# Optimization experiments

Hardware: AMD Instinct MI355X
Metric: run time of the kernel (lower is better)

## Reference

```python
import jax, jax.numpy as jnp
import numpy as np

EPS = 1e-18
MARGIN = 0.2  # hp.margin (cancels: positive/positive == 1)
BIAS = 1.0    # hp.bias


def setup_inputs() -> dict:
    key = jax.random.key(0)
    k1, k2, k3, k4 = jax.random.split(key, 4)
    B, T, D = 32, 256, 256  # T == D required by the broadcast in Ecos_sim
    return {
        "pre_VF": jax.random.normal(k1, (B, T, D), dtype=jnp.float32),
        "pre_AF": jax.random.normal(k2, (B, T, D), dtype=jnp.float32),
        "back_VF": jax.random.normal(k3, (B, T, D), dtype=jnp.float32),
        "back_AF": jax.random.normal(k4, (B, T, D), dtype=jnp.float32),
    }


def _direction_loss(V, A):
    """For each anchor i: log(1 + sum_{j != i} exp(sim(V_i, A_j))).

    sim(V_i, A_j)[t, s] = (V_i @ A_j.T)[t, s] / (||V_i||_F * colnorm(A_j)[s])
    (faithful to Ecos_sim: scalar Frobenius norm for V, per-column norm for A,
    broadcast along the last axis; positive/positive == 1 exactly, so the
    positive term and margin cancel.)
    """
    B = V.shape[0]
    # upper[i,j,t,s] = <V[i,t,:], A[j,s,:]>
    upper = jnp.einsum("itd,jsd->ijts", V, A)
    v_norm = jnp.sqrt(jnp.sum(V ** 2, axis=(1, 2)) + EPS)      # [B]
    a_norm = jnp.sqrt(jnp.sum(A ** 2, axis=1) + EPS)           # [B, D]
    sim = upper / (v_norm[:, None, None, None] * a_norm[None, :, None, :])
    e_sim = jnp.exp(sim)                                        # [B,B,T,T]
    idx = jnp.arange(B)
    down = e_sim.sum(axis=1) - e_sim[idx, idx]                  # exclude j == i
    rows = jnp.log(1.0 + down)                                  # [B,T,T]
    return rows.reshape(-1, rows.shape[-1])                     # cat along dim 0


def reference(pre_VF, pre_AF, back_VF, back_AF):
    sim_back_V = _direction_loss(back_VF, back_AF)
    sim_back_A = _direction_loss(back_AF, back_VF)
    return -(1.0 / BIAS) * (sim_back_V + sim_back_A)
```

## Files before the change

kernel.cpp:

```cpp
#include <hip/hip_runtime.h>
#include <cstdint>

#define R_TOT 8192
#define KD    256
#define SLOT  ((size_t)R_TOT * KD)
#define IVN_OFF  0
#define ICN_OFF  256
#define CSQ_OFF  (ICN_OFF + 65536)
#define MATS_OFF (CSQ_OFF + 524288)

typedef float f32x4 __attribute__((ext_vector_type(4)));
typedef long  lx2   __attribute__((ext_vector_type(2)));

__device__ __forceinline__ void glds16(const void* g, void* l){
  __builtin_amdgcn_global_load_lds((const __attribute__((address_space(1))) uint32_t*)g,
                                   (__attribute__((address_space(3))) uint32_t*)l, 16, 0, 0);
}

__global__ void cast_ns_k(const float* __restrict__ V, const float* __restrict__ A,
                          unsigned char* __restrict__ mats, float* __restrict__ csq){
  const int tc = blockIdx.x, j = blockIdx.y, ten = blockIdx.z;
  const int tid = threadIdx.x;
  const int g    = tid & 31;
  const int tsub = tid >> 5;
  const int q    = ((g >> 3) << 2) | (g & 3);
  const int half = (g >> 2) & 1;
  const float* X = (ten ? A : V) + (size_t)j * 65536;
  unsigned char* M = mats + (size_t)ten * SLOT + (size_t)j * 65536;
  float cs[8];
  #pragma unroll
  for (int e = 0; e < 8; ++e) cs[e] = 0.f;
  #pragma unroll
  for (int tt = 0; tt < 4; ++tt){
    const int t = tc * 32 + tt * 8 + tsub;
    const float4 p0 = *(const float4*)(X + t * 256 + g * 8);
    const float4 p1 = *(const float4*)(X + t * 256 + g * 8 + 4);
    cs[0] += p0.x * p0.x; cs[1] += p0.y * p0.y; cs[2] += p0.z * p0.z; cs[3] += p0.w * p0.w;
    cs[4] += p1.x * p1.x; cs[5] += p1.y * p1.y; cs[6] += p1.z * p1.z; cs[7] += p1.w * p1.w;
    int d0 = __builtin_amdgcn_cvt_pk_fp8_f32(p0.x, p0.y, 0, false);
    d0     = __builtin_amdgcn_cvt_pk_fp8_f32(p0.z, p0.w, d0, true);
    int d1 = __builtin_amdgcn_cvt_pk_fp8_f32(p1.x, p1.y, 0, false);
    d1     = __builtin_amdgcn_cvt_pk_fp8_f32(p1.z, p1.w, d1, true);
    int2 o; o.x = d0; o.y = d1;
    *(int2*)(M + (size_t)t * 256 + (((q ^ (t & 15)) << 4) | (half << 3))) = o;
  }
  __shared__ float red[8][256];
  #pragma unroll
  for (int e = 0; e < 8; ++e) red[tsub][g * 8 + e] = cs[e];
  __syncthreads();
  float s = 0.f;
  #pragma unroll
  for (int gg = 0; gg < 8; ++gg) s += red[gg][tid];
  csq[(size_t)((tc * 2 + ten) * 32 + j) * 256 + tid] = s;
}

__global__ void nreduce_k(const float* __restrict__ csq, float* __restrict__ ivn,
                          float* __restrict__ icn){
  const int j = blockIdx.x, ten = blockIdx.y, s = threadIdx.x;
  float c = 0.f;
  #pragma unroll
  for (int tc = 0; tc < 8; ++tc)
    c += csq[(size_t)((tc * 2 + ten) * 32 + j) * 256 + s];
  icn[ten * 8192 + j * 256 + s] = rsqrtf(c + 1e-18f);
  __shared__ float red[256];
  red[s] = c; __syncthreads();
  for (int off = 128; off > 0; off >>= 1){
    if (s < off) red[s] += red[s + off];
    __syncthreads();
  }
  if (s == 0) ivn[ten * 32 + j] = rsqrtf(red[0] + 1e-18f);
}

__global__ __launch_bounds__(256, 4) void gemm_both_k(const unsigned char* __restrict__ mats,
                                                      const float* __restrict__ ivn,
                                                      const float* __restrict__ icn,
                                                      float* __restrict__ out){
  __shared__ __align__(16) char smem[16384];
  const int tid  = threadIdx.x;
  const int lane = tid & 63;
  const int w    = tid >> 6;
  const int wm   = (w & 1) * 32;
  const int wn   = (w >> 1) * 16;
  const int wno  = wn << 8;
  const int lm   = lane & 15;
  const int kh   = lane >> 4;
  const int s0   = blockIdx.x * 32;
  const int rb   = blockIdx.y;
  const int r0   = rb * 64;
  const int ib   = rb >> 2;

  int a4[4];
  {
    const int base  = lm * 256 + ((kh ^ (lm & 3)) << 4);
    const int base2 = base ^ ((lm >> 2) << 6);
    #pragma unroll
    for (int t = 0; t < 4; ++t) a4[t] = base2 ^ (t << 6);
  }

  f32x4 accd[2][2];
  #pragma unroll
  for (int d = 0; d < 2; ++d)
    #pragma unroll
    for (int mi = 0; mi < 2; ++mi)
      accd[d][mi] = f32x4{0.f, 0.f, 0.f, 0.f};

  #pragma unroll
  for (int dir = 0; dir < 2; ++dir){
    const unsigned char* rowmat = mats + (size_t)dir * SLOT;
    const unsigned char* colmat = mats + (size_t)(1 - dir) * SLOT;
    const float sivn = ivn[dir * 32 + ib] * 1.44269504088896340736f;
    const float* icnb = icn + (size_t)(1 - dir) * 8192 + s0 + wn + lm;

    lx2 afr[2][4];
    #pragma unroll
    for (int mi = 0; mi < 2; ++mi){
      const unsigned char* rp = rowmat + (size_t)(r0 + wm + mi * 16 + lm) * 256;
      #pragma unroll
      for (int t = 0; t < 4; ++t)
        afr[mi][t] = *(const lx2*)(rp + (((((t << 2) | kh)) ^ lm) << 4));
    }
    #pragma unroll
    for (int mi = 0; mi < 2; ++mi)
      #pragma unroll
      for (int t = 0; t < 4; ++t)
        asm volatile("" : "+v"(afr[mi][t]));

    {
      const int j0 = (ib == 0) ? 1 : 0;
      const unsigned char* src = colmat + ((size_t)j0 * 256 + s0) * 256;
      #pragma unroll
      for (int c = 0; c < 2; ++c)
        glds16(src + (size_t)(c * 256 + tid) * 16, smem + (c * 256 + w * 64) * 16);
    }
    __syncthreads();

    for (int jj = 0; jj < 31; ++jj){
      const int j = jj + (jj >= ib ? 1 : 0);
      if (jj < 30){
        const int jn = (jj + 1) + ((jj + 1) >= ib ? 1 : 0);
        const unsigned char* src = colmat + ((size_t)jn * 256 + s0) * 256;
        char* dst = smem + (((jj + 1) & 1) << 13);
        #pragma unroll
        for (int c = 0; c < 2; ++c)
          glds16(src + (size_t)(c * 256 + tid) * 16, dst + (c * 256 + w * 64) * 16);
      }

      const float csc = sivn * icnb[j * 256];

      const char* rbuf = smem + ((jj & 1) << 13);
      f32x4 S[2];
      S[0] = f32x4{0.f, 0.f, 0.f, 0.f};
      S[1] = f32x4{0.f, 0.f, 0.f, 0.f};

      #pragma unroll
      for (int t = 0; t < 4; ++t){
        lx2 b = *(const lx2*)(rbuf + a4[t] + wno);
        S[0] = __builtin_amdgcn_mfma_f32_16x16x32_fp8_fp8(afr[0][t][0], b[0], S[0], 0, 0, 0);
        S[1] = __builtin_amdgcn_mfma_f32_16x16x32_fp8_fp8(afr[1][t][0], b[0], S[1], 0, 0, 0);
        S[0] = __builtin_amdgcn_mfma_f32_16x16x32_fp8_fp8(afr[0][t][1], b[1], S[0], 0, 0, 0);
        S[1] = __builtin_amdgcn_mfma_f32_16x16x32_fp8_fp8(afr[1][t][1], b[1], S[1], 0, 0, 0);
      }
      #pragma unroll
      for (int mi = 0; mi < 2; ++mi)
        #pragma unroll
        for (int r = 0; r < 4; ++r)
          accd[dir][mi][r] += __builtin_amdgcn_exp2f(S[mi][r] * csc);

      __syncthreads();
    }
  }

  float* ebuf = (float*)smem;
  #pragma unroll
  for (int mi = 0; mi < 2; ++mi){
    const int n = wn + lm;
    #pragma unroll
    for (int r = 0; r < 4; ++r){
      const int m = wm + mi * 16 + (kh << 2) + r;
      const float p0 = accd[0][mi][r], p1 = accd[1][mi][r];
      ebuf[m * 36 + n] = -(__logf(1.f + p0) + __logf(1.f + p1));
    }
  }
  __syncthreads();
  #pragma unroll
  for (int p = 0; p < 2; ++p){
    const int i   = tid + p * 256;
    const int row = i >> 3;
    const int c4  = i & 7;
    *(f32x4*)(&out[(size_t)(r0 + row) * 256 + s0 + c4 * 4]) = *(const f32x4*)(&ebuf[row * 36 + c4 * 4]);
  }
}

extern "C" void kernel_launch(void* const* d_in, const int* in_sizes, int n_in,
                              void* d_out, int out_size, void* d_ws, size_t ws_size,
                              hipStream_t stream){
  const float* V = (const float*)d_in[2];
  const float* A = (const float*)d_in[3];
  float* out = (float*)d_out;
  float* ivn = (float*)((char*)d_ws + IVN_OFF);
  float* icn = (float*)((char*)d_ws + ICN_OFF);
  float* csq = (float*)((char*)d_ws + CSQ_OFF);
  unsigned char* mats = (unsigned char*)((char*)d_ws + MATS_OFF);

  cast_ns_k<<<dim3(8, 32, 2), 256, 0, stream>>>(V, A, mats, csq);
  nreduce_k<<<dim3(32, 2), 256, 0, stream>>>(csq, ivn, icn);
  gemm_both_k<<<dim3(8, 128), 256, 0, stream>>>(mats, ivn, icn, out);
}
```

Measured before the change: 133.8 us.

## Fuse both similarity directions into a single j-loop with joint A/V tile staging

The two direction passes, V rows against A columns and A rows against V columns, now share one 31-iteration loop. Each iteration stages both the A and V column tiles into a doubled shared-memory buffer and issues eight independent MFMA chains instead of four. Both directions' row fragments stay resident in registers for the whole loop. This halves the number of loop iterations and barriers and gives the scheduler more independent MFMA and exp work to overlap with loads. The cost is twice the shared memory (32KB) and more registers per thread, which may lower occupancy under launch_bounds(256,4).

```diff
diff --git a/kernel.cpp b/kernel.cpp
--- a/kernel.cpp
+++ b/kernel.cpp
@@ -75,7 +75,7 @@
                                                       const float* __restrict__ ivn,
                                                       const float* __restrict__ icn,
                                                       float* __restrict__ out){
-  __shared__ __align__(16) char smem[16384];
+  __shared__ __align__(16) char smem[32768];
   const int tid  = threadIdx.x;
   const int lane = tid & 63;
   const int w    = tid >> 6;
@@ -89,6 +89,32 @@
   const int r0   = rb * 64;
   const int ib   = rb >> 2;
 
+  const unsigned char* Vq = mats;
+  const unsigned char* Aq = mats + SLOT;
+  const float l2e = 1.44269504088896340736f;
+  const float sivn0 = ivn[ib] * l2e;
+  const float sivn1 = ivn[32 + ib] * l2e;
+  const float* icn0 = icn + 8192 + s0 + wn + lm;
+  const float* icn1 = icn +        s0 + wn + lm;
+
+  lx2 afr[2][2][4];
+  #pragma unroll
+  for (int d = 0; d < 2; ++d)
+    #pragma unroll
+    for (int mi = 0; mi < 2; ++mi){
+      const unsigned char* rp = (d ? Aq : Vq) + (size_t)(r0 + wm + mi * 16 + lm) * 256;
+      #pragma unroll
+      for (int t = 0; t < 4; ++t)
+        afr[d][mi][t] = *(const lx2*)(rp + (((((t << 2) | kh)) ^ lm) << 4));
+    }
+  #pragma unroll
+  for (int d = 0; d < 2; ++d)
+    #pragma unroll
+    for (int mi = 0; mi < 2; ++mi)
+      #pragma unroll
+      for (int t = 0; t < 4; ++t)
+        asm volatile("" : "+v"(afr[d][mi][t]));
+
   int a4[4];
   {
     const int base  = lm * 256 + ((kh ^ (lm & 3)) << 4);
@@ -104,70 +130,67 @@
     for (int mi = 0; mi < 2; ++mi)
       accd[d][mi] = f32x4{0.f, 0.f, 0.f, 0.f};
 
-  #pragma unroll
-  for (int dir = 0; dir < 2; ++dir){
-    const unsigned char* rowmat = mats + (size_t)dir * SLOT;
-    const unsigned char* colmat = mats + (size_t)(1 - dir) * SLOT;
-    const float sivn = ivn[dir * 32 + ib] * 1.44269504088896340736f;
-    const float* icnb = icn + (size_t)(1 - dir) * 8192 + s0 + wn + lm;
-
-    lx2 afr[2][4];
-    #pragma unroll
-    for (int mi = 0; mi < 2; ++mi){
-      const unsigned char* rp = rowmat + (size_t)(r0 + wm + mi * 16 + lm) * 256;
-      #pragma unroll
-      for (int t = 0; t < 4; ++t)
-        afr[mi][t] = *(const lx2*)(rp + (((((t << 2) | kh)) ^ lm) << 4));
+  {
+    const int j0 = (ib == 0) ? 1 : 0;
+    const unsigned char* sA = Aq + ((size_t)j0 * 256 + s0) * 256;
+    const unsigned char* sV = Vq + ((size_t)j0 * 256 + s0) * 256;
+    #pragma unroll
+    for (int c = 0; c < 2; ++c)
+      glds16(sA + (size_t)(c * 256 + tid) * 16, smem + (c * 256 + w * 64) * 16);
+    #pragma unroll
+    for (int c = 0; c < 2; ++c)
+      glds16(sV + (size_t)(c * 256 + tid) * 16, smem + 8192 + (c * 256 + w * 64) * 16);
+  }
+  __syncthreads();
+
+  for (int jj = 0; jj < 31; ++jj){
+    const int j = jj + (jj >= ib ? 1 : 0);
+    if (jj < 30){
+      const int jn = (jj + 1) + ((jj + 1) >= ib ? 1 : 0);
+      const unsigned char* sA = Aq + ((size_t)jn * 256 + s0) * 256;
+      const unsigned char* sV = Vq + ((size_t)jn * 256 + s0) * 256;
+      char* dst = smem + (((jj + 1) & 1) << 14);
+      #pragma unroll
+      for (int c = 0; c < 2; ++c)
+        glds16(sA + (size_t)(c * 256 + tid) * 16, dst + (c * 256 + w * 64) * 16);
+      #pragma unroll
+      for (int c = 0; c < 2; ++c)
+        glds16(sV + (size_t)(c * 256 + tid) * 16, dst + 8192 + (c * 256 + w * 64) * 16);
+    }
+
+    const float csc0 = sivn0 * icn0[j * 256];
+    const float csc1 = sivn1 * icn1[j * 256];
+
+    const char* rbuf = smem + ((jj & 1) << 14);
+    f32x4 S[2][2];
+    #pragma unroll
+    for (int d = 0; d < 2; ++d)
+      #pragma unroll
+      for (int mi = 0; mi < 2; ++mi)
+        S[d][mi] = f32x4{0.f, 0.f, 0.f, 0.f};
+
+    #pragma unroll
+    for (int t = 0; t < 4; ++t){
+      lx2 ba = *(const lx2*)(rbuf + wno + a4[t]);
+      lx2 bv = *(const lx2*)(rbuf + 8192 + wno + a4[t]);
+      S[0][0] = __builtin_amdgcn_mfma_f32_16x16x32_fp8_fp8(afr[0][0][t][0], ba[0], S[0][0], 0, 0, 0);
+      S[0][1] = __builtin_amdgcn_mfma_f32_16x16x32_fp8_fp8(afr[0][1][t][0], ba[0], S[0][1], 0, 0, 0);
+      S[1][0] = __builtin_amdgcn_mfma_f32_16x16x32_fp8_fp8(afr[1][0][t][0], bv[0], S[1][0], 0, 0, 0);
+      S[1][1] = __builtin_amdgcn_mfma_f32_16x16x32_fp8_fp8(afr[1][1][t][0], bv[0], S[1][1], 0, 0, 0);
+      S[0][0] = __builtin_amdgcn_mfma_f32_16x16x32_fp8_fp8(afr[0][0][t][1], ba[1], S[0][0], 0, 0, 0);
+      S[0][1] = __builtin_amdgcn_mfma_f32_16x16x32_fp8_fp8(afr[0][1][t][1], ba[1], S[0][1], 0, 0, 0);
+      S[1][0] = __builtin_amdgcn_mfma_f32_16x16x32_fp8_fp8(afr[1][0][t][1], bv[1], S[1][0], 0, 0, 0);
+      S[1][1] = __builtin_amdgcn_mfma_f32_16x16x32_fp8_fp8(afr[1][1][t][1], bv[1], S[1][1], 0, 0, 0);
     }
     #pragma unroll
     for (int mi = 0; mi < 2; ++mi)
       #pragma unroll
-      for (int t = 0; t < 4; ++t)
-        asm volatile("" : "+v"(afr[mi][t]));
-
-    {
-      const int j0 = (ib == 0) ? 1 : 0;
-      const unsigned char* src = colmat + ((size_t)j0 * 256 + s0) * 256;
-      #pragma unroll
-      for (int c = 0; c < 2; ++c)
-        glds16(src + (size_t)(c * 256 + tid) * 16, smem + (c * 256 + w * 64) * 16);
-    }
+      for (int r = 0; r < 4; ++r){
+        accd[0][mi][r] += __builtin_amdgcn_exp2f(S[0][mi][r] * csc0);
+        accd[1][mi][r] += __builtin_amdgcn_exp2f(S[1][mi][r] * csc1);
+      }
+
     __syncthreads();
-
-    for (int jj = 0; jj < 31; ++jj){
-      const int j = jj + (jj >= ib ? 1 : 0);
-      if (jj < 30){
-        const int jn = (jj + 1) + ((jj + 1) >= ib ? 1 : 0);
-        const unsigned char* src = colmat + ((size_t)jn * 256 + s0) * 256;
-        char* dst = smem + (((jj + 1) & 1) << 13);
-        #pragma unroll
-        for (int c = 0; c < 2; ++c)
-          glds16(src + (size_t)(c * 256 + tid) * 16, dst + (c * 256 + w * 64) * 16);
-      }
-
-      const float csc = sivn * icnb[j * 256];
-
-      const char* rbuf = smem + ((jj & 1) << 13);
-      f32x4 S[2];
-      S[0] = f32x4{0.f, 0.f, 0.f, 0.f};
-      S[1] = f32x4{0.f, 0.f, 0.f, 0.f};
-
-      #pragma unroll
-      for (int t = 0; t < 4; ++t){
-        lx2 b = *(const lx2*)(rbuf + a4[t] + wno);
-        S[0] = __builtin_amdgcn_mfma_f32_16x16x32_fp8_fp8(afr[0][t][0], b[0], S[0], 0, 0, 0);
-        S[1] = __builtin_amdgcn_mfma_f32_16x16x32_fp8_fp8(afr[1][t][0], b[0], S[1], 0, 0, 0);
-        S[0] = __builtin_amdgcn_mfma_f32_16x16x32_fp8_fp8(afr[0][t][1], b[1], S[0], 0, 0, 0);
-        S[1] = __builtin_amdgcn_mfma_f32_16x16x32_fp8_fp8(afr[1][t][1], b[1], S[1], 0, 0, 0);
-      }
-      #pragma unroll
-      for (int mi = 0; mi < 2; ++mi)
-        #pragma unroll
-        for (int r = 0; r < 4; ++r)
-          accd[dir][mi][r] += __builtin_amdgcn_exp2f(S[mi][r] * csc);
-
-      __syncthreads();
-    }
   }
 
   float* ebuf = (float*)smem;
```

Result: no change. 132.9 us (-0.7%).

## Split directions across warps with per-warp private LDS double buffers

Applied to the files above, without the earlier changes.

The two loss directions are now computed concurrently by different warp pairs instead of sequentially by all four warps. Each warp holds all 64 rows of A fragments (4x4 registers) and streams its own 16-column B tile into a private double-buffered LDS region, which removes the block-wide __syncthreads from the 31-iteration loop. The two partial log terms are combined through shared memory at the end. In exchange, LDS doubles to 32 KB and register pressure rises, which may reduce occupancy. Without a barrier, each warp still relies on the async global-to-LDS load completing before it reads the buffer.

```diff
diff --git a/kernel.cpp b/kernel.cpp
--- a/kernel.cpp
+++ b/kernel.cpp
@@ -75,13 +75,12 @@
                                                       const float* __restrict__ ivn,
                                                       const float* __restrict__ icn,
                                                       float* __restrict__ out){
-  __shared__ __align__(16) char smem[16384];
+  __shared__ __align__(16) char smem[32768];
   const int tid  = threadIdx.x;
   const int lane = tid & 63;
   const int w    = tid >> 6;
-  const int wm   = (w & 1) * 32;
-  const int wn   = (w >> 1) * 16;
-  const int wno  = wn << 8;
+  const int dir  = w >> 1;
+  const int wn   = (w & 1) * 16;
   const int lm   = lane & 15;
   const int kh   = lane >> 4;
   const int s0   = blockIdx.x * 32;
@@ -89,6 +88,26 @@
   const int r0   = rb * 64;
   const int ib   = rb >> 2;
 
+  const unsigned char* rowmat = mats + (size_t)dir * SLOT;
+  const unsigned char* colmat = mats + (size_t)(1 - dir) * SLOT;
+  const float sivn = ivn[dir * 32 + ib] * 1.44269504088896340736f;
+  const float* icnb = icn + (size_t)(1 - dir) * 8192 + s0 + wn + lm;
+
+  lx2 afr[4][4];
+  #pragma unroll
+  for (int mi = 0; mi < 4; ++mi){
+    const unsigned char* rp = rowmat + (size_t)(r0 + mi * 16 + lm) * 256;
+    #pragma unroll
+    for (int t = 0; t < 4; ++t)
+      afr[mi][t] = *(const lx2*)(rp + (((((t << 2) | kh)) ^ lm) << 4));
+  }
+  #pragma unroll
+  for (int mi = 0; mi < 4; ++mi)
+    #pragma unroll
+    for (int t = 0; t < 4; ++t)
+      asm volatile("" : "+v"(afr[mi][t]));
+
+  char* wbase = smem + w * 8192;
   int a4[4];
   {
     const int base  = lm * 256 + ((kh ^ (lm & 3)) << 4);
@@ -96,89 +115,68 @@
     #pragma unroll
     for (int t = 0; t < 4; ++t) a4[t] = base2 ^ (t << 6);
   }
-
-  f32x4 accd[2][2];
-  #pragma unroll
-  for (int d = 0; d < 2; ++d)
-    #pragma unroll
-    for (int mi = 0; mi < 2; ++mi)
-      accd[d][mi] = f32x4{0.f, 0.f, 0.f, 0.f};
-
-  #pragma unroll
-  for (int dir = 0; dir < 2; ++dir){
-    const unsigned char* rowmat = mats + (size_t)dir * SLOT;
-    const unsigned char* colmat = mats + (size_t)(1 - dir) * SLOT;
-    const float sivn = ivn[dir * 32 + ib] * 1.44269504088896340736f;
-    const float* icnb = icn + (size_t)(1 - dir) * 8192 + s0 + wn + lm;
-
-    lx2 afr[2][4];
-    #pragma unroll
-    for (int mi = 0; mi < 2; ++mi){
-      const unsigned char* rp = rowmat + (size_t)(r0 + wm + mi * 16 + lm) * 256;
+  const int lo16 = lane * 16;
+
+  f32x4 acc[4];
+  #pragma unroll
+  for (int mi = 0; mi < 4; ++mi)
+    acc[mi] = f32x4{0.f, 0.f, 0.f, 0.f};
+
+  {
+    const int j0 = (ib == 0) ? 1 : 0;
+    const unsigned char* src = colmat + ((size_t)j0 * 256 + s0 + wn) * 256;
+    #pragma unroll
+    for (int c = 0; c < 4; ++c)
+      glds16(src + c * 1024 + lo16, wbase + c * 1024 + lo16);
+  }
+
+  for (int jj = 0; jj < 31; ++jj){
+    const int j = jj + (jj >= ib ? 1 : 0);
+    if (jj < 30){
+      const int jn = (jj + 1) + ((jj + 1) >= ib ? 1 : 0);
+      const unsigned char* src = colmat + ((size_t)jn * 256 + s0 + wn) * 256;
+      char* dst = wbase + (((jj + 1) & 1) << 12);
       #pragma unroll
-      for (int t = 0; t < 4; ++t)
-        afr[mi][t] = *(const lx2*)(rp + (((((t << 2) | kh)) ^ lm) << 4));
+      for (int c = 0; c < 4; ++c)
+        glds16(src + c * 1024 + lo16, dst + c * 1024 + lo16);
     }
-    #pragma unroll
-    for (int mi = 0; mi < 2; ++mi)
+
+    const float csc = sivn * icnb[j * 256];
+
+    const char* rbuf = wbase + ((jj & 1) << 12);
+    f32x4 S[4];
+    #pragma unroll
+    for (int mi = 0; mi < 4; ++mi)
+      S[mi] = f32x4{0.f, 0.f, 0.f, 0.f};
+
+    #pragma unroll
+    for (int t = 0; t < 4; ++t){
+      lx2 b = *(const lx2*)(rbuf + a4[t]);
+      S[0] = __builtin_amdgcn_mfma_f32_16x16x32_fp8_fp8(afr[0][t][0], b[0], S[0], 0, 0, 0);
+      S[1] = __builtin_amdgcn_mfma_f32_16x16x32_fp8_fp8(afr[1][t][0], b[0], S[1], 0, 0, 0);
+      S[2] = __builtin_amdgcn_mfma_f32_16x16x32_fp8_fp8(afr[2][t][0], b[0], S[2], 0, 0, 0);
+      S[3] = __builtin_amdgcn_mfma_f32_16x16x32_fp8_fp8(afr[3][t][0], b[0], S[3], 0, 0, 0);
+      S[0] = __builtin_amdgcn_mfma_f32_16x16x32_fp8_fp8(afr[0][t][1], b[1], S[0], 0, 0, 0);
+      S[1] = __builtin_amdgcn_mfma_f32_16x16x32_fp8_fp8(afr[1][t][1], b[1], S[1], 0, 0, 0);
+      S[2] = __builtin_amdgcn_mfma_f32_16x16x32_fp8_fp8(afr[2][t][1], b[1], S[2], 0, 0, 0);
+      S[3] = __builtin_amdgcn_mfma_f32_16x16x32_fp8_fp8(afr[3][t][1], b[1], S[3], 0, 0, 0);
+    }
+    #pragma unroll
+    for (int mi = 0; mi < 4; ++mi)
       #pragma unroll
-      for (int t = 0; t < 4; ++t)
-        asm volatile("" : "+v"(afr[mi][t]));
-
-    {
-      const int j0 = (ib == 0) ? 1 : 0;
-      const unsigned char* src = colmat + ((size_t)j0 * 256 + s0) * 256;
-      #pragma unroll
-      for (int c = 0; c < 2; ++c)
-        glds16(src + (size_t)(c * 256 + tid) * 16, smem + (c * 256 + w * 64) * 16);
-    }
-    __syncthreads();
-
-    for (int jj = 0; jj < 31; ++jj){
-      const int j = jj + (jj >= ib ? 1 : 0);
-      if (jj < 30){
-        const int jn = (jj + 1) + ((jj + 1) >= ib ? 1 : 0);
-        const unsigned char* src = colmat + ((size_t)jn * 256 + s0) * 256;
-        char* dst = smem + (((jj + 1) & 1) << 13);
-        #pragma unroll
-        for (int c = 0; c < 2; ++c)
-          glds16(src + (size_t)(c * 256 + tid) * 16, dst + (c * 256 + w * 64) * 16);
-      }
-
-      const float csc = sivn * icnb[j * 256];
-
-      const char* rbuf = smem + ((jj & 1) << 13);
-      f32x4 S[2];
-      S[0] = f32x4{0.f, 0.f, 0.f, 0.f};
-      S[1] = f32x4{0.f, 0.f, 0.f, 0.f};
-
-      #pragma unroll
-      for (int t = 0; t < 4; ++t){
-        lx2 b = *(const lx2*)(rbuf + a4[t] + wno);
-        S[0] = __builtin_amdgcn_mfma_f32_16x16x32_fp8_fp8(afr[0][t][0], b[0], S[0], 0, 0, 0);
-        S[1] = __builtin_amdgcn_mfma_f32_16x16x32_fp8_fp8(afr[1][t][0], b[0], S[1], 0, 0, 0);
-        S[0] = __builtin_amdgcn_mfma_f32_16x16x32_fp8_fp8(afr[0][t][1], b[1], S[0], 0, 0, 0);
-        S[1] = __builtin_amdgcn_mfma_f32_16x16x32_fp8_fp8(afr[1][t][1], b[1], S[1], 0, 0, 0);
-      }
-      #pragma unroll
-      for (int mi = 0; mi < 2; ++mi)
-        #pragma unroll
-        for (int r = 0; r < 4; ++r)
-          accd[dir][mi][r] += __builtin_amdgcn_exp2f(S[mi][r] * csc);
-
-      __syncthreads();
-    }
-  }
-
+      for (int r = 0; r < 4; ++r)
+        acc[mi][r] += __builtin_amdgcn_exp2f(S[mi][r] * csc);
+  }
+
+  __syncthreads();
   float* ebuf = (float*)smem;
   #pragma unroll
-  for (int mi = 0; mi < 2; ++mi){
+  for (int mi = 0; mi < 4; ++mi){
     const int n = wn + lm;
     #pragma unroll
     for (int r = 0; r < 4; ++r){
-      const int m = wm + mi * 16 + (kh << 2) + r;
-      const float p0 = accd[0][mi][r], p1 = accd[1][mi][r];
-      ebuf[m * 36 + n] = -(__logf(1.f + p0) + __logf(1.f + p1));
+      const int m = mi * 16 + (kh << 2) + r;
+      ebuf[(dir * 64 + m) * 36 + n] = __logf(1.f + acc[mi][r]);
     }
   }
   __syncthreads();
@@ -187,7 +185,12 @@
     const int i   = tid + p * 256;
     const int row = i >> 3;
     const int c4  = i & 7;
-    *(f32x4*)(&out[(size_t)(r0 + row) * 256 + s0 + c4 * 4]) = *(const f32x4*)(&ebuf[row * 36 + c4 * 4]);
+    const f32x4 e0 = *(const f32x4*)(&ebuf[row * 36 + c4 * 4]);
+    const f32x4 e1 = *(const f32x4*)(&ebuf[(64 + row) * 36 + c4 * 4]);
+    f32x4 o;
+    #pragma unroll
+    for (int e = 0; e < 4; ++e) o[e] = -(e0[e] + e1[e]);
+    *(f32x4*)(&out[(size_t)(r0 + row) * 256 + s0 + c4 * 4]) = o;
   }
 }
 
```

After: 129.0 us. -3.6%, faster.
